# Optimization experiments

Hardware: AMD Instinct MI355X
Metric: run time of the kernel (lower is better)

Reference implementation:

```python
import jax, jax.numpy as jnp
import numpy as np

D_MODEL = 1024
N_HEADS = 16
D_HEAD = D_MODEL // N_HEADS


def setup_inputs() -> dict:
    key = jax.random.key(0)
    ks = jax.random.split(key, 9)
    s = 1.0 / np.sqrt(D_MODEL)
    x = jax.random.normal(ks[0], (2, 2048, D_MODEL), dtype=jnp.float32)
    Wq = jax.random.uniform(ks[1], (D_MODEL, D_MODEL), jnp.float32, -s, s)
    bq = jax.random.uniform(ks[2], (D_MODEL,), jnp.float32, -s, s)
    Wk = jax.random.uniform(ks[3], (D_MODEL, D_MODEL), jnp.float32, -s, s)
    bk = jax.random.uniform(ks[4], (D_MODEL,), jnp.float32, -s, s)
    Wv = jax.random.uniform(ks[5], (D_MODEL, D_MODEL), jnp.float32, -s, s)
    bv = jax.random.uniform(ks[6], (D_MODEL,), jnp.float32, -s, s)
    Wo = jax.random.uniform(ks[7], (D_MODEL, D_MODEL), jnp.float32, -s, s)
    bo = jax.random.uniform(ks[8], (D_MODEL,), jnp.float32, -s, s)
    return {"x": x, "Wq": Wq, "bq": bq, "Wk": Wk, "bk": bk,
            "Wv": Wv, "bv": bv, "Wo": Wo, "bo": bo}


def reference(x, Wq, bq, Wk, bk, Wv, bv, Wo, bo):
    B, T, _ = x.shape
    # projections: (B, T, d_model) -> (B, H, T, d_head)
    def split_heads(y):
        return y.reshape(B, T, N_HEADS, D_HEAD).transpose(0, 2, 1, 3)
    Q = split_heads(x @ Wq + bq)
    K = split_heads(x @ Wk + bk)
    V = split_heads(x @ Wv + bv)
    scores = jnp.einsum('bhqd,bhkd->bhqk', Q, K) / jnp.sqrt(jnp.float32(D_HEAD))
    causal = jnp.tril(jnp.ones((T, T), dtype=bool))  # allowed positions
    scores = jnp.where(causal, scores, -jnp.inf)
    attn = jax.nn.softmax(scores, axis=-1)
    out = jnp.einsum('bhqk,bhkd->bhqd', attn, V)
    out = out.transpose(0, 2, 1, 3).reshape(B, T, D_MODEL)
    return out @ Wo + bo
```

## Files before the change

### kernel.cpp

```cpp
#include <hip/hip_runtime.h>

typedef unsigned short u16;
typedef unsigned int u32;

#define DM 1024
#define NH 16
#define DH 64
#define BB 2
#define TT 2048

#define SCLQ 0.18033688f

using frag8  = __attribute__((ext_vector_type(8))) short;
using bf16x8 = __attribute__((ext_vector_type(8))) __bf16;
using f32x4  = __attribute__((ext_vector_type(4))) float;

__device__ inline u16 f2bf(float f) {
  union { float f; u32 u; } v; v.f = f;
  u32 r = v.u + 0x7fffu + ((v.u >> 16) & 1u);
  return (u16)(r >> 16);
}

__device__ inline f32x4 mfma_bf16(frag8 a, frag8 b, f32x4 c) {
  return __builtin_amdgcn_mfma_f32_16x16x32_bf16(
      __builtin_bit_cast(bf16x8, a), __builtin_bit_cast(bf16x8, b), c, 0, 0, 0);
}

__device__ inline void gld16(void* lds, const void* g) {
  __builtin_amdgcn_global_load_lds(
      (const __attribute__((address_space(1))) void*)g,
      (__attribute__((address_space(3))) void*)lds, 16, 0, 0);
}

__device__ inline int swi(int row, int chunk) {
  return row * 64 + ((chunk ^ (row & 7)) << 3);
}

__global__ __launch_bounds__(256) void cvt_x_kernel(const float* __restrict__ X,
                                                    u16* __restrict__ Y) {
  int i = blockIdx.x * 256 + threadIdx.x;
  float4 v = ((const float4*)X)[i];
  ushort4 o;
  o.x = f2bf(v.x); o.y = f2bf(v.y); o.z = f2bf(v.z); o.w = f2bf(v.w);
  ((ushort4*)Y)[i] = o;
}

__global__ __launch_bounds__(256) void transpose_w_kernel(
    const float* __restrict__ W0, const float* __restrict__ W1,
    const float* __restrict__ W2, const float* __restrict__ W3,
    u16* __restrict__ O0, u16* __restrict__ O1,
    u16* __restrict__ O2, u16* __restrict__ O3) {
  const float* W; u16* Ot;
  switch (blockIdx.z) {
    case 0: W = W0; Ot = O0; break;
    case 1: W = W1; Ot = O1; break;
    case 2: W = W2; Ot = O2; break;
    default: W = W3; Ot = O3; break;
  }
  __shared__ u16 Ls[64][72];
  int tid = threadIdx.x;
  int n0 = blockIdx.x * 64;
  int k0 = blockIdx.y * 64;
#pragma unroll
  for (int p = 0; p < 4; ++p) {
    int id = tid + p * 256;
    int row = id >> 4;
    int c4 = (id & 15) * 4;
    float4 v = *(const float4*)&W[(size_t)(k0 + row) * DM + n0 + c4];
    ushort4 o; o.x = f2bf(v.x); o.y = f2bf(v.y); o.z = f2bf(v.z); o.w = f2bf(v.w);
    *(ushort4*)&Ls[row][c4] = o;
  }
  __syncthreads();
#pragma unroll
  for (int p = 0; p < 4; ++p) {
    int id = tid + p * 256;
    int row = id >> 4;
    int c4 = (id & 15) * 4;
    ushort4 o;
    o.x = Ls[c4 + 0][row]; o.y = Ls[c4 + 1][row];
    o.z = Ls[c4 + 2][row]; o.w = Ls[c4 + 3][row];
    *(ushort4*)&Ot[(size_t)(n0 + row) * DM + k0 + c4] = o;
  }
}

__global__ __launch_bounds__(256, 3) void gemm_qkv_kernel(
    const u16* __restrict__ A, const u16* __restrict__ Bt,
    const float* __restrict__ b0, const float* __restrict__ b1,
    const float* __restrict__ b2,
    u16* __restrict__ QK, u16* __restrict__ Vb) {
  constexpr int K = 1024;
  __shared__ u16 As[2][4096];
  __shared__ u16 Bs[2][4096];
  int tid = threadIdx.x;
  int lane = tid & 63, w = tid >> 6;
  int qd = lane >> 4, ln = lane & 15;
  int wm = (w & 1) * 64, wn = (w >> 1) * 64;
  int m0 = blockIdx.y * 128, n0 = blockIdx.x * 128;
  f32x4 z = {0.f, 0.f, 0.f, 0.f};
  f32x4 acc[4][4];
#pragma unroll
  for (int mi = 0; mi < 4; ++mi)
#pragma unroll
    for (int ni = 0; ni < 4; ++ni) acc[mi][ni] = z;

  const u16* ga = A + (size_t)(m0 + w * 32 + (lane >> 2)) * K + (lane & 3) * 8;
  const u16* gb = Bt + (size_t)(n0 + w * 32 + (lane >> 2)) * K + (lane & 3) * 8;

  gld16(&As[0][w * 1024],       ga);
  gld16(&As[0][w * 1024 + 512], ga + 16 * K);
  gld16(&Bs[0][w * 1024],       gb);
  gld16(&Bs[0][w * 1024 + 512], gb + 16 * K);

  for (int k0 = 0; k0 < K; k0 += 32) {
    int cur = (k0 >> 5) & 1;
    __syncthreads();
    if (k0 + 32 < K) {
      int nb = cur ^ 1;
      gld16(&As[nb][w * 1024],       ga + k0 + 32);
      gld16(&As[nb][w * 1024 + 512], ga + k0 + 32 + 16 * K);
      gld16(&Bs[nb][w * 1024],       gb + k0 + 32);
      gld16(&Bs[nb][w * 1024 + 512], gb + k0 + 32 + 16 * K);
    }
    frag8 af[4], bfr[4];
#pragma unroll
    for (int mi = 0; mi < 4; ++mi)
      af[mi] = *(const frag8*)&As[cur][(wm + mi * 16 + ln) * 32 + qd * 8];
#pragma unroll
    for (int ni = 0; ni < 4; ++ni)
      bfr[ni] = *(const frag8*)&Bs[cur][(wn + ni * 16 + ln) * 32 + qd * 8];
#pragma unroll
    for (int mi = 0; mi < 4; ++mi)
#pragma unroll
      for (int ni = 0; ni < 4; ++ni)
        acc[mi][ni] = mfma_bf16(af[mi], bfr[ni], acc[mi][ni]);
  }

#pragma unroll
  for (int ni = 0; ni < 4; ++ni) {
    int col = n0 + wn + ni * 16 + ln;
    if (col < 2048) {
      bool isq = col < 1024;
      float bias = isq ? b0[col] : b1[col - 1024];
#pragma unroll
      for (int mi = 0; mi < 4; ++mi) {
        int row = m0 + wm + mi * 16 + qd * 4;
#pragma unroll
        for (int r = 0; r < 4; ++r) {
          float v = acc[mi][ni][r] + bias;
          if (isq) v *= SCLQ;
          QK[(size_t)(row + r) * 2048 + col] = f2bf(v);
        }
      }
    } else {
      int c2 = col - 2048;
      float bias = b2[c2];
#pragma unroll
      for (int mi = 0; mi < 4; ++mi) {
        int row = m0 + wm + mi * 16 + qd * 4;
#pragma unroll
        for (int r = 0; r < 4; ++r)
          Vb[(size_t)(row + r) * 1024 + c2] = f2bf(acc[mi][ni][r] + bias);
      }
    }
  }
}

__global__ __launch_bounds__(256) void gemm_out_kernel(
    const u16* __restrict__ A, const u16* __restrict__ Bt,
    const float* __restrict__ b0, float* __restrict__ Cf) {
  constexpr int K = 1024;
  __shared__ u16 As[2][4096];
  __shared__ u16 Bs[2][2048];
  int tid = threadIdx.x;
  int lane = tid & 63, w = tid >> 6;
  int qd = lane >> 4, ln = lane & 15;
  int m0 = blockIdx.y * 128, n0 = blockIdx.x * 64;
  f32x4 z = {0.f, 0.f, 0.f, 0.f};
  f32x4 acc[2][4];
#pragma unroll
  for (int mi = 0; mi < 2; ++mi)
#pragma unroll
    for (int ni = 0; ni < 4; ++ni) acc[mi][ni] = z;

  const u16* ga = A + (size_t)(m0 + w * 32 + (lane >> 2)) * K + (lane & 3) * 8;
  const u16* gb = Bt + (size_t)(n0 + w * 16 + (lane >> 2)) * K + (lane & 3) * 8;

  gld16(&As[0][w * 1024],       ga);
  gld16(&As[0][w * 1024 + 512], ga + 16 * K);
  gld16(&Bs[0][w * 512],        gb);

  for (int k0 = 0; k0 < K; k0 += 32) {
    int cur = (k0 >> 5) & 1;
    __syncthreads();
    if (k0 + 32 < K) {
      int nb = cur ^ 1;
      gld16(&As[nb][w * 1024],       ga + k0 + 32);
      gld16(&As[nb][w * 1024 + 512], ga + k0 + 32 + 16 * K);
      gld16(&Bs[nb][w * 512],        gb + k0 + 32);
    }
    frag8 af[2], bfr[4];
#pragma unroll
    for (int mi = 0; mi < 2; ++mi)
      af[mi] = *(const frag8*)&As[cur][(w * 32 + mi * 16 + ln) * 32 + qd * 8];
#pragma unroll
    for (int ni = 0; ni < 4; ++ni)
      bfr[ni] = *(const frag8*)&Bs[cur][(ni * 16 + ln) * 32 + qd * 8];
#pragma unroll
    for (int mi = 0; mi < 2; ++mi)
#pragma unroll
      for (int ni = 0; ni < 4; ++ni)
        acc[mi][ni] = mfma_bf16(af[mi], bfr[ni], acc[mi][ni]);
  }

#pragma unroll
  for (int ni = 0; ni < 4; ++ni) {
    int col = n0 + ni * 16 + ln;
    float bias = b0[col];
#pragma unroll
    for (int mi = 0; mi < 2; ++mi) {
      int row = m0 + w * 32 + mi * 16 + qd * 4;
#pragma unroll
      for (int r = 0; r < 4; ++r)
        Cf[(size_t)(row + r) * 1024 + col] = acc[mi][ni][r] + bias;
    }
  }
}

__global__ __launch_bounds__(256) void transpose_v_kernel(const u16* __restrict__ V,
                                                          u16* __restrict__ Vt) {
  int bh = blockIdx.y;
  int b = bh >> 4, h = bh & 15;
  int t0 = blockIdx.x * 64;
  __shared__ u16 Ls[64][72];
  int tid = threadIdx.x;
#pragma unroll
  for (int p = 0; p < 2; ++p) {
    int id = tid + p * 256;
    int row = id >> 3, seg = id & 7;
    *(uint4*)&Ls[row][seg * 8] =
        *(const uint4*)&V[(size_t)(b * TT + t0 + row) * DM + h * DH + seg * 8];
  }
  __syncthreads();
#pragma unroll
  for (int p = 0; p < 2; ++p) {
    int id = tid + p * 256;
    int d = id >> 3, seg = id & 7;
    union { u16 s[8]; uint4 v; } tmp;
#pragma unroll
    for (int j = 0; j < 8; ++j) tmp.s[j] = Ls[seg * 8 + j][d];
    *(uint4*)&Vt[(size_t)(bh * DH + d) * TT + t0 + seg * 8] = tmp.v;
  }
}

__global__ __launch_bounds__(256, 3) void flash4_kernel(const u16* __restrict__ QK,
                                                        const u16* __restrict__ Vt,
                                                        u16* __restrict__ O) {
  int pj = blockIdx.x;
  int bh = blockIdx.y;
  int b = bh >> 4, h = bh & 15;
  int qtA = pj, qtB = 31 - pj;
  int q0A = qtA * 64, q0B = qtB * 64;
  __shared__ u16 Ks[2 * 4096];
  __shared__ u16 Vs[2 * 4096];
  __shared__ u16 PsA[4096];
  __shared__ u16 PsB[4096];
  int tid = threadIdx.x;
  int lane = tid & 63, w = tid >> 6;
  int qd = lane >> 4, ln = lane & 15;

  frag8 qfA[2], qfB[2];
#pragma unroll
  for (int kk = 0; kk < 2; ++kk) {
    qfA[kk] = *(const frag8*)&QK[(size_t)(b * TT + q0A + w * 16 + ln) * 2048 +
                                 h * 64 + kk * 32 + qd * 8];
    qfB[kk] = *(const frag8*)&QK[(size_t)(b * TT + q0B + w * 16 + ln) * 2048 +
                                 h * 64 + kk * 32 + qd * 8];
  }

  int lr = lane >> 3, lc = (lane & 7) ^ lr;
  const u16* KgA = &QK[(size_t)(b * TT + w * 16 + lr) * 2048 + 1024 + h * 64 + lc * 8];
  const u16* KgB = KgA + 8 * 2048;
  const u16* VgA = &Vt[(size_t)(bh * 64 + w * 16 + lr) * 2048 + lc * 8];
  const u16* VgB = VgA + 8 * 2048;
  int ldsw = w * 1024;

  int nkt = qtB + 1;

  gld16(&Ks[ldsw],       KgA);
  gld16(&Ks[ldsw + 512], KgB);
  gld16(&Vs[ldsw],       VgA);
  gld16(&Vs[ldsw + 512], VgB);

  float lA = 0.f, lB = 0.f;
  f32x4 z = {0.f, 0.f, 0.f, 0.f};
  f32x4 oA[4] = {z, z, z, z};
  f32x4 oB[4] = {z, z, z, z};

  for (int kt = 0; kt < nkt; ++kt) {
    int cur = kt & 1;
    int cb = cur * 4096;
    __syncthreads();

    if (kt + 1 < nkt) {
      int nb = (cur ^ 1) * 4096;
      size_t ko = (size_t)(kt + 1) * 64 * 2048;
      int vo = (kt + 1) * 64;
      gld16(&Ks[nb + ldsw],       KgA + ko);
      gld16(&Ks[nb + ldsw + 512], KgB + ko);
      gld16(&Vs[nb + ldsw],       VgA + vo);
      gld16(&Vs[nb + ldsw + 512], VgB + vo);
    }

    bool actA  = (kt <= qtA);
    bool diagA = (kt == qtA);
    bool diagB = (kt == qtB);

    f32x4 sA[4] = {z, z, z, z};
    f32x4 sB[4] = {z, z, z, z};
#pragma unroll
    for (int mi = 0; mi < 4; ++mi) {
      bool skipB = diagB && (mi > w);
      bool doA = actA && !(diagA && (mi > w));
      if (skipB && !doA) continue;
#pragma unroll
      for (int kk = 0; kk < 2; ++kk) {
        frag8 ak = *(const frag8*)&Ks[cb + swi(mi * 16 + ln, 4 * kk + qd)];
        if (!skipB) sB[mi] = mfma_bf16(ak, qfB[kk], sB[mi]);
        if (doA)    sA[mi] = mfma_bf16(ak, qfA[kk], sA[mi]);
      }
    }

    auto softmax_store = [&](f32x4* s, bool diag, u16* Ps, float& lacc) {
#pragma unroll
      for (int mi = 0; mi < 4; ++mi) {
        int pb = swi(w * 16 + ln, 2 * mi + (qd >> 1)) + (qd & 1) * 4;
        if (diag && mi > w) {
          uint2 zz; zz.x = 0u; zz.y = 0u;
          *(uint2*)&Ps[pb] = zz;
          continue;
        }
        float p0 = __builtin_amdgcn_exp2f(s[mi][0]);
        float p1 = __builtin_amdgcn_exp2f(s[mi][1]);
        float p2 = __builtin_amdgcn_exp2f(s[mi][2]);
        float p3 = __builtin_amdgcn_exp2f(s[mi][3]);
        if (diag && mi == w) {
          p0 = (qd * 4 + 0 <= ln) ? p0 : 0.f;
          p1 = (qd * 4 + 1 <= ln) ? p1 : 0.f;
          p2 = (qd * 4 + 2 <= ln) ? p2 : 0.f;
          p3 = (qd * 4 + 3 <= ln) ? p3 : 0.f;
        }
        lacc += (p0 + p1) + (p2 + p3);
        u32 u0 = __builtin_bit_cast(u32, p0) + 0x8000u;
        u32 u1 = __builtin_bit_cast(u32, p1) + 0x8000u;
        u32 u2 = __builtin_bit_cast(u32, p2) + 0x8000u;
        u32 u3 = __builtin_bit_cast(u32, p3) + 0x8000u;
        uint2 pk;
        pk.x = __builtin_amdgcn_perm(u1, u0, 0x07060302u);
        pk.y = __builtin_amdgcn_perm(u3, u2, 0x07060302u);
        *(uint2*)&Ps[pb] = pk;
      }
    };
    softmax_store(sB, diagB, PsB, lB);
    if (actA) softmax_store(sA, diagA, PsA, lA);

#pragma unroll
    for (int kk = 0; kk < 2; ++kk) {
      if (diagB && kk == 1 && w < 2) continue;
      frag8 bpB = *(const frag8*)&PsB[swi(w * 16 + ln, 4 * kk + qd)];
      frag8 bpA;
      if (actA) bpA = *(const frag8*)&PsA[swi(w * 16 + ln, 4 * kk + qd)];
#pragma unroll
      for (int mi = 0; mi < 4; ++mi) {
        frag8 av = *(const frag8*)&Vs[cb + swi(mi * 16 + ln, 4 * kk + qd)];
        oB[mi] = mfma_bf16(av, bpB, oB[mi]);
        if (actA) oA[mi] = mfma_bf16(av, bpA, oA[mi]);
      }
    }
  }

  lA += __shfl_xor(lA, 16); lA += __shfl_xor(lA, 32);
  lB += __shfl_xor(lB, 16); lB += __shfl_xor(lB, 32);
  float rlA = 1.0f / lA, rlB = 1.0f / lB;

#pragma unroll
  for (int mi = 0; mi < 4; ++mi) {
    ushort4 ov;
    ov.x = f2bf(oA[mi][0] * rlA); ov.y = f2bf(oA[mi][1] * rlA);
    ov.z = f2bf(oA[mi][2] * rlA); ov.w = f2bf(oA[mi][3] * rlA);
    *(ushort4*)&O[(size_t)(b * TT + q0A + w * 16 + ln) * DM + h * 64 + mi * 16 + qd * 4] = ov;
    ov.x = f2bf(oB[mi][0] * rlB); ov.y = f2bf(oB[mi][1] * rlB);
    ov.z = f2bf(oB[mi][2] * rlB); ov.w = f2bf(oB[mi][3] * rlB);
    *(ushort4*)&O[(size_t)(b * TT + q0B + w * 16 + ln) * DM + h * 64 + mi * 16 + qd * 4] = ov;
  }
}

extern "C" void kernel_launch(void* const* d_in, const int* in_sizes, int n_in,
                              void* d_out, int out_size, void* d_ws, size_t ws_size,
                              hipStream_t stream) {
  const float* x  = (const float*)d_in[0];
  const float* Wq = (const float*)d_in[1];
  const float* bq = (const float*)d_in[2];
  const float* Wk = (const float*)d_in[3];
  const float* bk = (const float*)d_in[4];
  const float* Wv = (const float*)d_in[5];
  const float* bv = (const float*)d_in[6];
  const float* Wo = (const float*)d_in[7];
  const float* bo = (const float*)d_in[8];

  char* ws = (char*)d_ws;
  const size_t MB = 1ull << 20;
  u16* xbf  = (u16*)(ws + 0);
  u16* Wcat = (u16*)(ws + 8 * MB);
  u16* Wot  = (u16*)(ws + 14 * MB);
  u16* QKb  = (u16*)(ws + 16 * MB);
  u16* Vbb  = (u16*)(ws + 32 * MB);
  u16* Vtb  = (u16*)(ws + 40 * MB);
  u16* Ob   = (u16*)(ws + 48 * MB);

  cvt_x_kernel<<<4096, 256, 0, stream>>>(x, xbf);
  transpose_w_kernel<<<dim3(16, 16, 4), 256, 0, stream>>>(
      Wq, Wk, Wv, Wo, Wcat, Wcat + 1024 * 1024, Wcat + 2 * 1024 * 1024, Wot);
  gemm_qkv_kernel<<<dim3(24, 32), 256, 0, stream>>>(
      xbf, Wcat, bq, bk, bv, QKb, Vbb);
  transpose_v_kernel<<<dim3(32, 32), 256, 0, stream>>>(Vbb, Vtb);
  flash4_kernel<<<dim3(16, 32), 256, 0, stream>>>(QKb, Vtb, Ob);
  gemm_out_kernel<<<dim3(16, 32), 256, 0, stream>>>(Ob, Wot, bo, (float*)d_out);
}
```

Baseline: 211.6 us.

## Split paired-query-tile flash kernel into one tile per block with setprio

The attention kernel no longer pairs two query tiles (qt and 31-qt) per block sharing K/V loads. It now launches one block per 64-row query tile, so there are twice as many blocks, and it raises the occupancy hint from 3 to 4 blocks with a smaller LDS footprint. It also wraps the MFMA sections in s_setprio. This trades K/V reuse across the paired tiles and per-block load balance for more parallelism and occupancy, at the risk of a causal tail imbalance and doubled K/V traffic.

```diff
diff --git a/kernel.cpp b/kernel.cpp
--- a/kernel.cpp
+++ b/kernel.cpp
@@ -252,49 +252,43 @@
   }
 }
 
-__global__ __launch_bounds__(256, 3) void flash4_kernel(const u16* __restrict__ QK,
+__global__ __launch_bounds__(256, 4) void flash5_kernel(const u16* __restrict__ QK,
                                                         const u16* __restrict__ Vt,
                                                         u16* __restrict__ O) {
-  int pj = blockIdx.x;
+  int qt = blockIdx.x;
   int bh = blockIdx.y;
   int b = bh >> 4, h = bh & 15;
-  int qtA = pj, qtB = 31 - pj;
-  int q0A = qtA * 64, q0B = qtB * 64;
+  int q0 = qt * 64;
   __shared__ u16 Ks[2 * 4096];
   __shared__ u16 Vs[2 * 4096];
-  __shared__ u16 PsA[4096];
-  __shared__ u16 PsB[4096];
+  __shared__ u16 Ps[4096];
   int tid = threadIdx.x;
   int lane = tid & 63, w = tid >> 6;
   int qd = lane >> 4, ln = lane & 15;
 
-  frag8 qfA[2], qfB[2];
-#pragma unroll
-  for (int kk = 0; kk < 2; ++kk) {
-    qfA[kk] = *(const frag8*)&QK[(size_t)(b * TT + q0A + w * 16 + ln) * 2048 +
-                                 h * 64 + kk * 32 + qd * 8];
-    qfB[kk] = *(const frag8*)&QK[(size_t)(b * TT + q0B + w * 16 + ln) * 2048 +
-                                 h * 64 + kk * 32 + qd * 8];
-  }
+  frag8 qf[2];
+#pragma unroll
+  for (int kk = 0; kk < 2; ++kk)
+    qf[kk] = *(const frag8*)&QK[(size_t)(b * TT + q0 + w * 16 + ln) * 2048 +
+                                h * 64 + kk * 32 + qd * 8];
 
   int lr = lane >> 3, lc = (lane & 7) ^ lr;
-  const u16* KgA = &QK[(size_t)(b * TT + w * 16 + lr) * 2048 + 1024 + h * 64 + lc * 8];
-  const u16* KgB = KgA + 8 * 2048;
-  const u16* VgA = &Vt[(size_t)(bh * 64 + w * 16 + lr) * 2048 + lc * 8];
-  const u16* VgB = VgA + 8 * 2048;
+  const u16* Kg  = &QK[(size_t)(b * TT + w * 16 + lr) * 2048 + 1024 + h * 64 + lc * 8];
+  const u16* Kg2 = Kg + 8 * 2048;
+  const u16* Vg  = &Vt[(size_t)(bh * 64 + w * 16 + lr) * 2048 + lc * 8];
+  const u16* Vg2 = Vg + 8 * 2048;
   int ldsw = w * 1024;
 
-  int nkt = qtB + 1;
-
-  gld16(&Ks[ldsw],       KgA);
-  gld16(&Ks[ldsw + 512], KgB);
-  gld16(&Vs[ldsw],       VgA);
-  gld16(&Vs[ldsw + 512], VgB);
-
-  float lA = 0.f, lB = 0.f;
+  int nkt = qt + 1;
+
+  gld16(&Ks[ldsw],       Kg);
+  gld16(&Ks[ldsw + 512], Kg2);
+  gld16(&Vs[ldsw],       Vg);
+  gld16(&Vs[ldsw + 512], Vg2);
+
+  float l = 0.f;
   f32x4 z = {0.f, 0.f, 0.f, 0.f};
-  f32x4 oA[4] = {z, z, z, z};
-  f32x4 oB[4] = {z, z, z, z};
+  f32x4 o[4] = {z, z, z, z};
 
   for (int kt = 0; kt < nkt; ++kt) {
     int cur = kt & 1;
@@ -305,92 +299,80 @@
       int nb = (cur ^ 1) * 4096;
       size_t ko = (size_t)(kt + 1) * 64 * 2048;
       int vo = (kt + 1) * 64;
-      gld16(&Ks[nb + ldsw],       KgA + ko);
-      gld16(&Ks[nb + ldsw + 512], KgB + ko);
-      gld16(&Vs[nb + ldsw],       VgA + vo);
-      gld16(&Vs[nb + ldsw + 512], VgB + vo);
-    }
-
-    bool actA  = (kt <= qtA);
-    bool diagA = (kt == qtA);
-    bool diagB = (kt == qtB);
-
-    f32x4 sA[4] = {z, z, z, z};
-    f32x4 sB[4] = {z, z, z, z};
+      gld16(&Ks[nb + ldsw],       Kg + ko);
+      gld16(&Ks[nb + ldsw + 512], Kg2 + ko);
+      gld16(&Vs[nb + ldsw],       Vg + vo);
+      gld16(&Vs[nb + ldsw + 512], Vg2 + vo);
+    }
+
+    bool diag = (kt == qt);
+
+    f32x4 s[4] = {z, z, z, z};
+    __builtin_amdgcn_s_setprio(1);
 #pragma unroll
     for (int mi = 0; mi < 4; ++mi) {
-      bool skipB = diagB && (mi > w);
-      bool doA = actA && !(diagA && (mi > w));
-      if (skipB && !doA) continue;
+      if (diag && mi > w) continue;
 #pragma unroll
       for (int kk = 0; kk < 2; ++kk) {
         frag8 ak = *(const frag8*)&Ks[cb + swi(mi * 16 + ln, 4 * kk + qd)];
-        if (!skipB) sB[mi] = mfma_bf16(ak, qfB[kk], sB[mi]);
-        if (doA)    sA[mi] = mfma_bf16(ak, qfA[kk], sA[mi]);
-      }
-    }
-
-    auto softmax_store = [&](f32x4* s, bool diag, u16* Ps, float& lacc) {
-#pragma unroll
-      for (int mi = 0; mi < 4; ++mi) {
-        int pb = swi(w * 16 + ln, 2 * mi + (qd >> 1)) + (qd & 1) * 4;
-        if (diag && mi > w) {
-          uint2 zz; zz.x = 0u; zz.y = 0u;
-          *(uint2*)&Ps[pb] = zz;
-          continue;
-        }
-        float p0 = __builtin_amdgcn_exp2f(s[mi][0]);
-        float p1 = __builtin_amdgcn_exp2f(s[mi][1]);
-        float p2 = __builtin_amdgcn_exp2f(s[mi][2]);
-        float p3 = __builtin_amdgcn_exp2f(s[mi][3]);
-        if (diag && mi == w) {
-          p0 = (qd * 4 + 0 <= ln) ? p0 : 0.f;
-          p1 = (qd * 4 + 1 <= ln) ? p1 : 0.f;
-          p2 = (qd * 4 + 2 <= ln) ? p2 : 0.f;
-          p3 = (qd * 4 + 3 <= ln) ? p3 : 0.f;
-        }
-        lacc += (p0 + p1) + (p2 + p3);
-        u32 u0 = __builtin_bit_cast(u32, p0) + 0x8000u;
-        u32 u1 = __builtin_bit_cast(u32, p1) + 0x8000u;
-        u32 u2 = __builtin_bit_cast(u32, p2) + 0x8000u;
-        u32 u3 = __builtin_bit_cast(u32, p3) + 0x8000u;
-        uint2 pk;
-        pk.x = __builtin_amdgcn_perm(u1, u0, 0x07060302u);
-        pk.y = __builtin_amdgcn_perm(u3, u2, 0x07060302u);
-        *(uint2*)&Ps[pb] = pk;
-      }
-    };
-    softmax_store(sB, diagB, PsB, lB);
-    if (actA) softmax_store(sA, diagA, PsA, lA);
-
+        s[mi] = mfma_bf16(ak, qf[kk], s[mi]);
+      }
+    }
+    __builtin_amdgcn_s_setprio(0);
+
+#pragma unroll
+    for (int mi = 0; mi < 4; ++mi) {
+      int pb = swi(w * 16 + ln, 2 * mi + (qd >> 1)) + (qd & 1) * 4;
+      if (diag && mi > w) {
+        uint2 zz; zz.x = 0u; zz.y = 0u;
+        *(uint2*)&Ps[pb] = zz;
+        continue;
+      }
+      float p0 = __builtin_amdgcn_exp2f(s[mi][0]);
+      float p1 = __builtin_amdgcn_exp2f(s[mi][1]);
+      float p2 = __builtin_amdgcn_exp2f(s[mi][2]);
+      float p3 = __builtin_amdgcn_exp2f(s[mi][3]);
+      if (diag && mi == w) {
+        p0 = (qd * 4 + 0 <= ln) ? p0 : 0.f;
+        p1 = (qd * 4 + 1 <= ln) ? p1 : 0.f;
+        p2 = (qd * 4 + 2 <= ln) ? p2 : 0.f;
+        p3 = (qd * 4 + 3 <= ln) ? p3 : 0.f;
+      }
+      l += (p0 + p1) + (p2 + p3);
+      u32 u0 = __builtin_bit_cast(u32, p0) + 0x8000u;
+      u32 u1 = __builtin_bit_cast(u32, p1) + 0x8000u;
+      u32 u2 = __builtin_bit_cast(u32, p2) + 0x8000u;
+      u32 u3 = __builtin_bit_cast(u32, p3) + 0x8000u;
+      uint2 pk;
+      pk.x = __builtin_amdgcn_perm(u1, u0, 0x07060302u);
+      pk.y = __builtin_amdgcn_perm(u3, u2, 0x07060302u);
+      *(uint2*)&Ps[pb] = pk;
+    }
+
+    __builtin_amdgcn_s_setprio(1);
 #pragma unroll
     for (int kk = 0; kk < 2; ++kk) {
-      if (diagB && kk == 1 && w < 2) continue;
-      frag8 bpB = *(const frag8*)&PsB[swi(w * 16 + ln, 4 * kk + qd)];
-      frag8 bpA;
-      if (actA) bpA = *(const frag8*)&PsA[swi(w * 16 + ln, 4 * kk + qd)];
+      if (diag && kk == 1 && w < 2) continue;
+      frag8 bp = *(const frag8*)&Ps[swi(w * 16 + ln, 4 * kk + qd)];
 #pragma unroll
       for (int mi = 0; mi < 4; ++mi) {
         frag8 av = *(const frag8*)&Vs[cb + swi(mi * 16 + ln, 4 * kk + qd)];
-        oB[mi] = mfma_bf16(av, bpB, oB[mi]);
-        if (actA) oA[mi] = mfma_bf16(av, bpA, oA[mi]);
-      }
-    }
-  }
-
-  lA += __shfl_xor(lA, 16); lA += __shfl_xor(lA, 32);
-  lB += __shfl_xor(lB, 16); lB += __shfl_xor(lB, 32);
-  float rlA = 1.0f / lA, rlB = 1.0f / lB;
+        o[mi] = mfma_bf16(av, bp, o[mi]);
+      }
+    }
+    __builtin_amdgcn_s_setprio(0);
+  }
+
+  l += __shfl_xor(l, 16);
+  l += __shfl_xor(l, 32);
+  float rl = 1.0f / l;
 
 #pragma unroll
   for (int mi = 0; mi < 4; ++mi) {
     ushort4 ov;
-    ov.x = f2bf(oA[mi][0] * rlA); ov.y = f2bf(oA[mi][1] * rlA);
-    ov.z = f2bf(oA[mi][2] * rlA); ov.w = f2bf(oA[mi][3] * rlA);
-    *(ushort4*)&O[(size_t)(b * TT + q0A + w * 16 + ln) * DM + h * 64 + mi * 16 + qd * 4] = ov;
-    ov.x = f2bf(oB[mi][0] * rlB); ov.y = f2bf(oB[mi][1] * rlB);
-    ov.z = f2bf(oB[mi][2] * rlB); ov.w = f2bf(oB[mi][3] * rlB);
-    *(ushort4*)&O[(size_t)(b * TT + q0B + w * 16 + ln) * DM + h * 64 + mi * 16 + qd * 4] = ov;
+    ov.x = f2bf(o[mi][0] * rl); ov.y = f2bf(o[mi][1] * rl);
+    ov.z = f2bf(o[mi][2] * rl); ov.w = f2bf(o[mi][3] * rl);
+    *(ushort4*)&O[(size_t)(b * TT + q0 + w * 16 + ln) * DM + h * 64 + mi * 16 + qd * 4] = ov;
   }
 }
 
@@ -423,6 +405,6 @@
   gemm_qkv_kernel<<<dim3(24, 32), 256, 0, stream>>>(
       xbf, Wcat, bq, bk, bv, QKb, Vbb);
   transpose_v_kernel<<<dim3(32, 32), 256, 0, stream>>>(Vbb, Vtb);
-  flash4_kernel<<<dim3(16, 32), 256, 0, stream>>>(QKb, Vtb, Ob);
+  flash5_kernel<<<dim3(32, 32), 256, 0, stream>>>(QKb, Vtb, Ob);
   gemm_out_kernel<<<dim3(16, 32), 256, 0, stream>>>(Ob, Wot, bo, (float*)d_out);
 }
```

New measurement: 211.7 us. Within noise of the previous version (+0.0%).
